# Optimization experiments

Hardware: AMD Instinct MI355X
Metric: run time of the kernel (lower is better)

The kernel has to match this reference:

```python
import jax, jax.numpy as jnp
import numpy as np

B, S, D, H, NATT = 8, 512, 768, 256, 11  # batch, seq, d_model, gru hidden, n attention branches


def setup_inputs() -> dict:
    key = jax.random.key(0)
    ks = jax.random.split(key, 20)
    w = lambda k, shp, s=0.02: (jax.random.normal(k, shp, jnp.float32) * s)
    emb = w(ks[0], (7, D), 1.0).at[0].set(0.0)  # padding_idx=0 row is zero
    return {
        "essay_amlabel": jax.random.randint(ks[1], (B, S), 0, 7),
        "sequence_output": jax.random.normal(ks[2], (B, S, D), jnp.float32),
        "emb_table": emb,
        "Wq": w(ks[3], (NATT, D, D)), "bq": jnp.zeros((NATT, D), jnp.float32),
        "Wk": w(ks[4], (NATT, D, D)), "bk": jnp.zeros((NATT, D), jnp.float32),
        "Wv": w(ks[5], (NATT, D, D)), "bv": jnp.zeros((NATT, D), jnp.float32),
        "gru_Wih": w(ks[6], (2, 3 * H, D), 1.0 / np.sqrt(H)),
        "gru_Whh": w(ks[7], (2, 3 * H, H), 1.0 / np.sqrt(H)),
        "gru_bih": jnp.zeros((2, 3 * H), jnp.float32),
        "gru_bhh": jnp.zeros((2, 3 * H), jnp.float32),
        "W1": w(ks[8], (2 * H, 1)), "b1": jnp.zeros((1,), jnp.float32),
    }


def _gru_final_hidden(x, Wih, Whh, bih, bhh, reverse):
    # x: [N, S, D] -> final hidden [N, H] (PyTorch GRU equations)
    xp = jnp.einsum('nsd,hd->snh', x, Wih) + bih  # [S, N, 3H]

    def step(h, xt):
        gh = h @ Whh.T + bhh
        i_r, i_z, i_n = jnp.split(xt, 3, axis=-1)
        h_r, h_z, h_n = jnp.split(gh, 3, axis=-1)
        r = jax.nn.sigmoid(i_r + h_r)
        z = jax.nn.sigmoid(i_z + h_z)
        n = jnp.tanh(i_n + r * h_n)
        h_new = (1.0 - z) * n + z * h
        return h_new, None

    h0 = jnp.zeros((x.shape[0], Whh.shape[1]), x.dtype)
    h_final, _ = jax.lax.scan(step, h0, xp, reverse=reverse)
    return h_final


def reference(essay_amlabel, sequence_output, emb_table, Wq, bq, Wk, bk, Wv, bv,
              gru_Wih, gru_Whh, gru_bih, gru_bhh, W1, b1):
    am = emb_table[essay_amlabel]  # [B, S, D] queries
    # 11 independent attentions, num_heads=1, dropout=0 (eval) -> stack on axis k
    Q = jax.nn.relu(jnp.einsum('bsd,kde->kbse', am, Wq) + bq[:, None, None, :])
    K = jax.nn.relu(jnp.einsum('bsd,kde->kbse', sequence_output, Wk) + bk[:, None, None, :])
    V = jax.nn.relu(jnp.einsum('bsd,kde->kbse', sequence_output, Wv) + bv[:, None, None, :])
    scores = jnp.einsum('kbqd,kbmd->kbqm', Q, K) / jnp.sqrt(jnp.float32(D))
    attn = jax.nn.softmax(scores, axis=-1)
    qmask = jnp.sign(jnp.abs(jnp.sum(am, axis=-1)))  # [B, S]
    attn = attn * qmask[None, :, :, None]  # post-softmax query mask (as in source)
    out = jnp.einsum('kbqm,kbmd->kbqd', attn, V) + am[None]  # residual with queries
    eloutput = out + sequence_output[None]  # [11, B, S, D]
    gru_in = eloutput.reshape(NATT * B, S, D)
    h_f = _gru_final_hidden(gru_in, gru_Wih[0], gru_Whh[0], gru_bih[0], gru_bhh[0], False)
    h_b = _gru_final_hidden(gru_in, gru_Wih[1], gru_Whh[1], gru_bih[1], gru_bhh[1], True)
    final = jnp.concatenate([h_f, h_b], axis=-1)  # [11B, 2H]
    reshaped = final.reshape(NATT, B, 2 * H).transpose(1, 0, 2)  # [B, 11, 2H]
    logits = jax.nn.sigmoid(reshaped @ W1 + b1).squeeze(-1)  # [B, 11]
    return logits
```

## Files before the change

### kernel.cpp

```cpp
#include <hip/hip_runtime.h>
#include <hip/hip_bf16.h>
#include <hip/hip_fp16.h>
#include <math.h>

typedef __hip_bfloat16 bf16;
typedef __attribute__((ext_vector_type(8))) short short8;
typedef __attribute__((ext_vector_type(4))) float f32x4;

#define NATT 11
#define Bb 8
#define Ss 512
#define Dd 768
#define Hh 256
#define WSLICE 589824L

#if defined(__has_attribute)
#if __has_attribute(amdgpu_waves_per_eu)
#define WAVES22 __attribute__((amdgpu_waves_per_eu(2, 2)))
#else
#define WAVES22
#endif
#if __has_attribute(amdgpu_agpr_alloc)
#define NO_AGPR __attribute__((amdgpu_agpr_alloc(0)))
#else
#define NO_AGPR
#endif
#else
#define WAVES22
#define NO_AGPR
#endif

__device__ __forceinline__ void stf(float* p, float v) { *p = v; }
__device__ __forceinline__ void stf(bf16* p, float v) { *p = __float2bfloat16(v); }

__device__ __forceinline__ float blo(unsigned u) { return __uint_as_float(u << 16); }
__device__ __forceinline__ float bhi(unsigned u) { return __uint_as_float(u & 0xffff0000u); }
__device__ __forceinline__ float b2f(unsigned short u) { return __uint_as_float(((unsigned)u) << 16); }

__device__ __forceinline__ float ldg_any(const void* base, long idx, int flag) {
  if (flag) return ((const float*)base)[idx];
  return __bfloat162float(((const bf16*)base)[idx]);
}

__device__ __forceinline__ unsigned packh2(float a, float b) {
  __half2 hh = __floats2half2_rn(a, b);
  return __builtin_bit_cast(unsigned, hh);
}
__device__ __forceinline__ unsigned short f2h(float v) {
  __half h = __float2half(v);
  return __builtin_bit_cast(unsigned short, h);
}

typedef _Float16 f16x2 __attribute__((ext_vector_type(2)));

__device__ __forceinline__ float dot2u(unsigned a, unsigned b, float c) {
#if __has_builtin(__builtin_amdgcn_fdot2)
  return __builtin_amdgcn_fdot2(__builtin_bit_cast(f16x2, a),
                                __builtin_bit_cast(f16x2, b), c, false);
#else
  __half2 ah = __builtin_bit_cast(__half2, a);
  __half2 bh = __builtin_bit_cast(__half2, b);
  float2 af = __half22float2(ah), bf = __half22float2(bh);
  return c + af.x * bf.x + af.y * bf.y;
#endif
}

__device__ __forceinline__ float quad_sum(float v) {
#if __has_builtin(__builtin_amdgcn_update_dpp)
  int y = __builtin_amdgcn_update_dpp(0, __builtin_bit_cast(int, v), 0xB1, 0xF, 0xF, true);
  v += __builtin_bit_cast(float, y);
  y = __builtin_amdgcn_update_dpp(0, __builtin_bit_cast(int, v), 0x4E, 0xF, 0xF, true);
  v += __builtin_bit_cast(float, y);
  return v;
#else
  v += __shfl_xor(v, 1);
  v += __shfl_xor(v, 2);
  return v;
#endif
}

__device__ __forceinline__ void lds_barrier() {
  asm volatile("s_waitcnt lgkmcnt(0)\n\ts_barrier" ::: "memory");
}

__device__ __forceinline__ void load_lds16(const void* g, void* l) {
  __builtin_amdgcn_global_load_lds(
      (const __attribute__((address_space(1))) unsigned int*)g,
      (__attribute__((address_space(3))) unsigned int*)l, 16, 0, 0);
}

__global__ __launch_bounds__(64) void probe_kernel(
    const unsigned short* __restrict__ sequ, const unsigned* __restrict__ labu,
    int* __restrict__ flags)
{
  int t = threadIdx.x;
  int wild = 0;
#pragma unroll
  for (int i = 0; i < 4; i++) {
    unsigned short v = sequ[t + i * 64];
    int e = (v >> 7) & 0xFF;
    if (e < 90 || e > 160) wild++;
  }
  int nzodd = 0;
#pragma unroll
  for (int i = 0; i < 2; i++) {
    unsigned w = labu[(t + i * 64) * 2 + 1];
    if (w != 0) nzodd++;
  }
  for (int o = 32; o > 0; o >>= 1) {
    wild  += __shfl_down(wild, o);
    nzodd += __shfl_down(nzodd, o);
  }
  if (t == 0) {
    flags[0] = (wild > 32) ? 1 : 0;
    flags[1] = (nzodd == 0) ? 1 : 0;
  }
}

__global__ __launch_bounds__(256) void conv_seq_kernel(
    const void* __restrict__ seq, bf16* __restrict__ seqb,
    const int* __restrict__ flags)
{
  int flag = flags[0];
  long row = blockIdx.x;
#pragma unroll
  for (int i = 0; i < 3; i++) {
    long e = row * Dd + threadIdx.x + i * 256;
    seqb[e] = __float2bfloat16(ldg_any(seq, e, flag));
  }
}

__global__ __launch_bounds__(256) void convert_kernel(
    const void* __restrict__ src, bf16* __restrict__ dst, long n,
    const int* __restrict__ flags)
{
  int flag = flags[0];
  long i = (long)blockIdx.x * 256 + threadIdx.x;
  if (i < n) dst[i] = __float2bfloat16(ldg_any(src, i, flag));
}

__global__ __launch_bounds__(256) void smalls_kernel(
    const void* __restrict__ emb, const void* __restrict__ Wq,
    const void* __restrict__ bq, float* __restrict__ Qsmall,
    const int* __restrict__ flags)
{
  int flag = flags[0];
  __shared__ float embsh[7 * 768];
  __shared__ float psum[4][7][64];
  int z = blockIdx.y;
  int bx = blockIdx.x;
  int tid = threadIdx.x;
  int sub = tid >> 6, nl = tid & 63;
  for (int i = tid; i < 7 * 768; i += 256) embsh[i] = ldg_any(emb, i, flag);
  __syncthreads();
  int n = bx * 64 + nl;
  long base = (long)z * WSLICE;
  float acc[7] = {};
  int e0 = sub * 192;
  for (int e = e0; e < e0 + 192; e++) {
    float wv = ldg_any(Wq, base + (long)e * Dd + n, flag);
#pragma unroll
    for (int l = 0; l < 7; l++) acc[l] += embsh[l * 768 + e] * wv;
  }
#pragma unroll
  for (int l = 0; l < 7; l++) psum[sub][l][nl] = acc[l];
  __syncthreads();
  if (sub == 0) {
    float bv = ldg_any(bq, z * Dd + n, flag);
#pragma unroll
    for (int l = 0; l < 7; l++) {
      float v = psum[0][l][nl] + psum[1][l][nl] + psum[2][l][nl] + psum[3][l][nl] + bv;
      Qsmall[((long)z * 7 + l) * Dd + n] = fmaxf(v, 0.f);
    }
  }
}

__global__ __launch_bounds__(256) void emb_copy_kernel(
    const void* __restrict__ emb, bf16* __restrict__ outsm,
    float* __restrict__ qmask7, const int* __restrict__ flags)
{
  int flag = flags[0];
  int l = blockIdx.x;
  int t = threadIdx.x;
  float s = 0.f;
#pragma unroll
  for (int i = 0; i < 3; i++) {
    int e = t + i * 256;
    float v = ldg_any(emb, (long)l * Dd + e, flag);
    outsm[(long)(640 + l) * Dd + e] = __float2bfloat16(v);
    s += v;
  }
  for (int o = 32; o > 0; o >>= 1) s += __shfl_down(s, o);
  __shared__ float red[4];
  if ((t & 63) == 0) red[t >> 6] = s;
  __syncthreads();
  if (t == 0) {
    float tot = red[0] + red[1] + red[2] + red[3];
    qmask7[l] = (tot != 0.f) ? 1.f : 0.f;
  }
}

__global__ __launch_bounds__(256) void transpose2_kernel(
    const void* __restrict__ Wk, const void* __restrict__ Wv,
    bf16* __restrict__ WT, const int* __restrict__ flags)
{
  int flag = flags[0];
  __shared__ float tile[32][33];
  int z = blockIdx.z;
  int m = z >> 1, wsel = z & 1;
  const void* src = wsel ? Wv : Wk;
  long off = (long)m * WSLICE;
  bf16* dst = WT + (long)z * WSLICE;
  int kk0 = blockIdx.y * 32, n0 = blockIdx.x * 32;
  int tx = threadIdx.x & 31, ty = threadIdx.x >> 5;
#pragma unroll
  for (int i = 0; i < 4; i++)
    tile[ty + i * 8][tx] = ldg_any(src, off + (long)(kk0 + ty + i * 8) * Dd + n0 + tx, flag);
  __syncthreads();
#pragma unroll
  for (int i = 0; i < 4; i++)
    dst[(long)(n0 + ty + i * 8) * Dd + kk0 + tx] = __float2bfloat16(tile[tx][ty + i * 8]);
}

__device__ __forceinline__ void gemm_mfma_core(
    const bf16* __restrict__ Ab, long ldA,
    const bf16* __restrict__ Bbp, long ldB,
    bf16* As, bf16* Bs, int bm, int bn, int K,
    const void* bias, long bOff,
    void* C, long ldC, int cMode,
    float scale, int relu, int fflag)
{
  int tid = threadIdx.x;
  int lane = tid & 63, w = tid >> 6;
  int mo = (w & 1) * 64, no = (w >> 1) * 64;
  int l15 = lane & 15, q4 = lane >> 4;
  int gr = lane >> 2;
  int gs = (lane & 3) * 8;
  const bf16* aS0 = Ab + (long)(bm + w * 16 + gr) * ldA + gs;
  const bf16* aS1 = aS0 + 64 * ldA;
  const bf16* bS0 = Bbp + (long)(bn + w * 16 + gr) * ldB + gs;
  const bf16* bS1 = bS0 + 64 * ldB;
  bf16* aD0 = As + w * 512;
  bf16* aD1 = As + 2048 + w * 512;
  bf16* bD0 = Bs + w * 512;
  bf16* bD1 = Bs + 2048 + w * 512;

  f32x4 acc[4][4];
#pragma unroll
  for (int i = 0; i < 4; i++)
#pragma unroll
    for (int j = 0; j < 4; j++)
#pragma unroll
      for (int r = 0; r < 4; r++) acc[i][j][r] = 0.f;

  for (int k0 = 0; k0 < K; k0 += 32) {
    load_lds16(aS0, aD0);
    load_lds16(aS1, aD1);
    load_lds16(bS0, bD0);
    load_lds16(bS1, bD1);
    aS0 += 32; aS1 += 32; bS0 += 32; bS1 += 32;
    __syncthreads();
    short8 af[4], bfv[4];
#pragma unroll
    for (int i = 0; i < 4; i++)
      af[i] = *(const short8*)(As + (mo + i * 16 + l15) * 32 + q4 * 8);
#pragma unroll
    for (int j = 0; j < 4; j++)
      bfv[j] = *(const short8*)(Bs + (no + j * 16 + l15) * 32 + q4 * 8);
#pragma unroll
    for (int i = 0; i < 4; i++)
#pragma unroll
      for (int j = 0; j < 4; j++)
        acc[i][j] = __builtin_amdgcn_mfma_f32_16x16x32_bf16(af[i], bfv[j], acc[i][j], 0, 0, 0);
    __syncthreads();
  }

  float bsv[4];
#pragma unroll
  for (int j = 0; j < 4; j++) {
    int colg = bn + no + j * 16 + l15;
    bsv[j] = bias ? ldg_any(bias, bOff + colg, fflag) : 0.f;
  }

  if (cMode == 5) {
    unsigned short* tile = (unsigned short*)As;
    int cl = (no >> 6) * 16 + l15;
#pragma unroll
    for (int j = 0; j < 4; j++) {
      __syncthreads();
#pragma unroll
      for (int i = 0; i < 4; i++) {
#pragma unroll
        for (int r = 0; r < 4; r++) {
          float v = acc[i][j][r] * scale + bsv[j];
          if (relu) v = fmaxf(v, 0.f);
          tile[cl * 136 + mo + i * 16 + q4 * 4 + r] = f2h(v);
        }
      }
      __syncthreads();
#pragma unroll
      for (int uu = 0; uu < 2; uu++) {
        int u = tid + uu * 256;
        int c = u >> 4, mseg = u & 15;
        int colg = bn + (c >> 4) * 64 + j * 16 + (c & 15);
        uint2 v0 = *(const uint2*)(tile + c * 136 + mseg * 8);
        uint2 v1 = *(const uint2*)(tile + c * 136 + mseg * 8 + 4);
        uint4 pk; pk.x = v0.x; pk.y = v0.y; pk.z = v1.x; pk.w = v1.y;
        *(uint4*)((unsigned short*)C + (long)colg * ldC + bm + mseg * 8) = pk;
      }
    }
    return;
  }

#pragma unroll
  for (int i = 0; i < 4; i++) {
#pragma unroll
    for (int j = 0; j < 4; j++) {
      int colg = bn + no + j * 16 + l15;
#pragma unroll
      for (int r = 0; r < 4; r++) {
        int rowg = bm + mo + i * 16 + q4 * 4 + r;
        float v = acc[i][j][r] * scale + bsv[j];
        if (relu) v = fmaxf(v, 0.f);
        long off2 = (long)rowg * ldC + colg;
        if (cMode == 2)      ((float*)C)[off2] = v;
        else if (cMode == 3) ((unsigned short*)C)[off2] = f2h(v);
        else                 ((bf16*)C)[off2] = __float2bfloat16(v);
      }
    }
  }
}

__global__ __launch_bounds__(256, 2) void proj_kernel(
    const bf16* __restrict__ seqb, const bf16* __restrict__ WT,
    const void* __restrict__ bk, const void* __restrict__ bv,
    const bf16* __restrict__ WihB, const void* __restrict__ bih,
    unsigned short* __restrict__ Kb, unsigned short* __restrict__ Vt,
    bf16* __restrict__ seqW, const int* __restrict__ flags)
{
  __shared__ __align__(16) bf16 smem[8192];
  bf16* As = smem;
  bf16* Bs = smem + 4096;
  int z = blockIdx.z;
  if (z < 22) {
    int m = z >> 1, wsel = z & 1;
    const bf16* B = WT + (long)z * WSLICE;
    if (wsel == 0) {
      gemm_mfma_core(seqb, Dd, B, Dd, As, Bs, blockIdx.y * 128, blockIdx.x * 128, Dd,
                     bk, (long)m * Dd, Kb + (long)m * 4096 * Dd, Dd, 3, 1.f, 1, flags[0]);
    } else {
      gemm_mfma_core(seqb, Dd, B, Dd, As, Bs, blockIdx.y * 128, blockIdx.x * 128, Dd,
                     bv, (long)m * Dd, Vt + (long)m * Dd * 4096, 4096, 5, 1.f, 1, flags[0]);
    }
  } else {
    int dir = z - 22;
    gemm_mfma_core(seqb, Dd, WihB + (long)dir * WSLICE, Dd, As, Bs,
                   blockIdx.y * 128, blockIdx.x * 128, Dd,
                   bih, (long)dir * Dd, seqW + (long)dir * 4096 * Dd, Dd, 0,
                   1.f, 0, flags[0]);
  }
}

__global__ __launch_bounds__(256, 2) void pvw_kernel(
    const bf16* __restrict__ outsm, const bf16* __restrict__ WihB,
    float* __restrict__ PVW, const int* __restrict__ flags)
{
  __shared__ __align__(16) bf16 As[4096];
  __shared__ __align__(16) bf16 Bs[4096];
  int dir = blockIdx.z;
  gemm_mfma_core(outsm, Dd, WihB + (long)dir * WSLICE, Dd, As, Bs,
                 blockIdx.y * 128, blockIdx.x * 128, Dd,
                 nullptr, 0, PVW + (long)dir * 768 * Dd, Dd, 2, 1.f, 0, flags[0]);
}

__global__ __launch_bounds__(512, 2) void attn_kernel(
    const unsigned short* __restrict__ Kb, const unsigned short* __restrict__ Vt,
    const float* __restrict__ Qsmall, const float* __restrict__ qmask7,
    bf16* __restrict__ outsm, float scl)
{
  int blk = blockIdx.x;
  int k = blk >> 3, b = blk & 7;
  int tid = threadIdx.x;
  int lane = tid & 63, w = tid >> 6;
  __shared__ unsigned qs[7][384];
  __shared__ unsigned short ash[7][512];
  __shared__ float wred[8][7];
  __shared__ float gred[7];
  __shared__ float finv[7];
  for (int i = tid; i < 7 * 384; i += 512) {
    int l = i / 384, e2 = i - l * 384;
    const float* qp = Qsmall + ((long)k * 7 + l) * Dd + 2 * e2;
    qs[l][e2] = packh2(qp[0], qp[1]);
  }
  __syncthreads();
  const uint4* Krow = (const uint4*)(Kb + ((long)k * 4096 + b * 512 + tid) * Dd);
  float sc[7] = {};
  for (int e8 = 0; e8 < 96; e8++) {
    uint4 kv = Krow[e8];
#pragma unroll
    for (int l = 0; l < 7; l++) {
      sc[l] = dot2u(qs[l][e8 * 4],     kv.x, sc[l]);
      sc[l] = dot2u(qs[l][e8 * 4 + 1], kv.y, sc[l]);
      sc[l] = dot2u(qs[l][e8 * 4 + 2], kv.z, sc[l]);
      sc[l] = dot2u(qs[l][e8 * 4 + 3], kv.w, sc[l]);
    }
  }
#pragma unroll
  for (int l = 0; l < 7; l++) sc[l] *= scl;
#pragma unroll
  for (int l = 0; l < 7; l++) {
    float v = sc[l];
    for (int o = 32; o > 0; o >>= 1) v = fmaxf(v, __shfl_down(v, o));
    if (lane == 0) wred[w][l] = v;
  }
  __syncthreads();
  if (tid < 7) {
    float m = wred[0][tid];
#pragma unroll
    for (int i = 1; i < 8; i++) m = fmaxf(m, wred[i][tid]);
    gred[tid] = m;
  }
  __syncthreads();
  float ev[7];
#pragma unroll
  for (int l = 0; l < 7; l++) {
    ev[l] = __expf(sc[l] - gred[l]);
    float v = ev[l];
    for (int o = 32; o > 0; o >>= 1) v += __shfl_down(v, o);
    if (lane == 0) wred[w][l] = v;
  }
  __syncthreads();
  if (tid < 7) {
    float s = 0.f;
#pragma unroll
    for (int i = 0; i < 8; i++) s += wred[i][tid];
    finv[tid] = qmask7[tid] / s;
  }
  __syncthreads();
#pragma unroll
  for (int l = 0; l < 7; l++) ash[l][tid] = f2h(ev[l] * finv[l]);
  __syncthreads();
  for (int rep = 0; rep < 2; rep++) {
    int n = tid + rep * 512;
    if (n >= Dd) break;
    const uint4* Vrow = (const uint4*)(Vt + ((long)k * Dd + n) * 4096 + b * 512);
    float acc[7] = {};
    for (int m8 = 0; m8 < 64; m8++) {
      uint4 vv = Vrow[m8];
#pragma unroll
      for (int l = 0; l < 7; l++) {
        const unsigned* ap = (const unsigned*)&ash[l][0];
        acc[l] = dot2u(ap[m8 * 4],     vv.x, acc[l]);
        acc[l] = dot2u(ap[m8 * 4 + 1], vv.y, acc[l]);
        acc[l] = dot2u(ap[m8 * 4 + 2], vv.z, acc[l]);
        acc[l] = dot2u(ap[m8 * 4 + 3], vv.w, acc[l]);
      }
    }
#pragma unroll
    for (int l = 0; l < 7; l++)
      outsm[((long)blk * 7 + l) * Dd + n] = __float2bfloat16(acc[l]);
  }
}

__global__ __launch_bounds__(512) WAVES22 NO_AGPR void gru_kernel(
    const bf16* __restrict__ seqW,
    const float* __restrict__ PVW,
    const void* __restrict__ labels,
    const void* __restrict__ Whh, const void* __restrict__ bhh,
    float* __restrict__ hbuf, const int* __restrict__ flags)
{
  int flag = flags[0], lflag = flags[1];
  int idx = blockIdx.x;
  int dir = idx / 88, n = idx - dir * 88;
  int b = n & 7;
  int tid = threadIdx.x;
  int q = tid & 3, cg = tid >> 2;
  int hi = q >> 1;
  int ch = cg + hi * 128;
  int r0 = ch, r1 = 256 + ch, r2 = 512 + ch;

  unsigned w[6][32];
#pragma unroll
  for (int s = 0; s < 6; s++) {
    int row = (s >> 1) * 256 + cg + (s & 1) * 128;
    long base = ((long)dir * Dd + row) * Hh + q * 64;
    if (flag) {
      const float4* s4 = (const float4*)((const float*)Whh + base);
#pragma unroll
      for (int i = 0; i < 16; i++) {
        float4 v = s4[i];
        w[s][2 * i]     = packh2(v.x, v.y);
        w[s][2 * i + 1] = packh2(v.z, v.w);
      }
    } else {
      const uint4* s4 = (const uint4*)((const bf16*)Whh + base);
#pragma unroll
      for (int i = 0; i < 8; i++) {
        uint4 v = s4[i];
        w[s][4 * i]     = packh2(blo(v.x), bhi(v.x));
        w[s][4 * i + 1] = packh2(blo(v.y), bhi(v.y));
        w[s][4 * i + 2] = packh2(blo(v.z), bhi(v.z));
        w[s][4 * i + 3] = packh2(blo(v.w), bhi(v.w));
      }
    }
  }
  float bh0 = ldg_any(bhh, dir * Dd + r0, flag);
  float bh1 = ldg_any(bhh, dir * Dd + r1, flag);
  float bh2 = ldg_any(bhh, dir * Dd + r2, flag);

  __shared__ float rowsh[7 * 768];
  __shared__ int labsh[512];
  __shared__ __align__(16) unsigned short hsh[2][4 * 72];

  for (int i = tid; i < 7 * 768; i += 512) {
    int l = i / 768, row = i - l * 768;
    rowsh[i] = PVW[((long)dir * 768 + n * 7 + l) * Dd + row]
             + PVW[((long)dir * 768 + 640 + l) * Dd + row];
  }
  labsh[tid] = lflag ? (int)((const long long*)labels)[b * 512 + tid]
                     : ((const int*)labels)[b * 512 + tid];
  if (tid < 288) { hsh[0][tid] = 0; hsh[1][tid] = 0; }
  __syncthreads();

  const unsigned short* swu = (const unsigned short*)seqW
                            + ((long)dir * 4096 + b * 512) * Dd;
  int t0 = dir ? 511 : 0, t1 = dir ? 510 : 1, t2 = dir ? 509 : 2;
  unsigned short xs00 = swu[(long)t0 * Dd + r0];
  unsigned short xs01 = swu[(long)t0 * Dd + r1];
  unsigned short xs02 = swu[(long)t0 * Dd + r2];
  unsigned short xs10 = swu[(long)t1 * Dd + r0];
  unsigned short xs11 = swu[(long)t1 * Dd + r1];
  unsigned short xs12 = swu[(long)t1 * Dd + r2];
  unsigned short xs20 = swu[(long)t2 * Dd + r0];
  unsigned short xs21 = swu[(long)t2 * Dd + r1];
  unsigned short xs22 = swu[(long)t2 * Dd + r2];

  float hprev = 0.f;
  int hwaddr = (ch >> 6) * 72 + (ch & 63);
  for (int tt = 0; tt < Ss; tt++) {
    int t = dir ? 511 - tt : tt;
    int ttp = (tt + 3 < Ss) ? tt + 3 : Ss - 1;
    int tp = dir ? 511 - ttp : ttp;
    unsigned short xp0 = swu[(long)tp * Dd + r0];
    unsigned short xp1 = swu[(long)tp * Dd + r1];
    unsigned short xp2 = swu[(long)tp * Dd + r2];
    int lab = labsh[t];
    const float* rs = rowsh + lab * 768;
    float xr = rs[r0] + b2f(xs00);
    float xz = rs[r1] + b2f(xs01);
    float xn = rs[r2] + b2f(xs02);
    const uint4* hq = (const uint4*)(hsh[tt & 1] + q * 72);
    float a[6] = {};
#pragma unroll
    for (int jj = 0; jj < 8; jj++) {
      uint4 hv = hq[jj];
#pragma unroll
      for (int s = 0; s < 6; s++) {
        a[s] = dot2u(w[s][4 * jj],     hv.x, a[s]);
        a[s] = dot2u(w[s][4 * jj + 1], hv.y, a[s]);
        a[s] = dot2u(w[s][4 * jj + 2], hv.z, a[s]);
        a[s] = dot2u(w[s][4 * jj + 3], hv.w, a[s]);
      }
    }
#pragma unroll
    for (int s = 0; s < 6; s++) a[s] = quad_sum(a[s]);
    float ar = hi ? a[1] : a[0];
    float az = hi ? a[3] : a[2];
    float an = hi ? a[5] : a[4];
    float rg = 1.f / (1.f + __expf(-(xr + ar + bh0)));
    float zg = 1.f / (1.f + __expf(-(xz + az + bh1)));
    float targ = xn + rg * (an + bh2);
    float e2 = __expf(2.f * targ);
    float ng = 1.f - 2.f / (e2 + 1.f);
    float hnew = (1.f - zg) * ng + zg * hprev;
    hprev = hnew;
    if ((q & 1) == 0) hsh[(tt + 1) & 1][hwaddr] = f2h(hnew);
    lds_barrier();
    xs00 = xs10; xs01 = xs11; xs02 = xs12;
    xs10 = xs20; xs11 = xs21; xs12 = xs22;
    xs20 = xp0;  xs21 = xp1;  xs22 = xp2;
  }
  if ((q & 1) == 0) hbuf[((long)(dir * 88 + n)) * Hh + ch] = hprev;
}

__global__ __launch_bounds__(256) void head_kernel(
    const float* __restrict__ hbuf, const void* __restrict__ W1,
    const void* __restrict__ b1, void* __restrict__ out,
    const int* __restrict__ flags)
{
  int flag = flags[0];
  int n = blockIdx.x;
  int c = threadIdx.x;
  float v = hbuf[(long)n * Hh + c] * ldg_any(W1, c, flag)
          + hbuf[(long)(88 + n) * Hh + c] * ldg_any(W1, 256 + c, flag);
  for (int o = 32; o > 0; o >>= 1) v += __shfl_down(v, o);
  __shared__ float red[4];
  if ((c & 63) == 0) red[c >> 6] = v;
  __syncthreads();
  if (c == 0) {
    float s = red[0] + red[1] + red[2] + red[3] + ldg_any(b1, 0, flag);
    float sig = 1.f / (1.f + __expf(-s));
    int k = n / Bb, b = n - k * Bb;
    int o = b * NATT + k;
    if (flag) ((float*)out)[o] = sig;
    else      stf((bf16*)out + o, sig);
  }
}

extern "C" void kernel_launch(void* const* d_in, const int* in_sizes, int n_in,
                              void* d_out, int out_size, void* d_ws, size_t ws_size,
                              hipStream_t stream) {
  const void* labels = d_in[0];
  const void* seq  = d_in[1];
  const void* emb  = d_in[2];
  const void* Wq   = d_in[3];
  const void* bq   = d_in[4];
  const void* Wk   = d_in[5];
  const void* bk   = d_in[6];
  const void* Wv   = d_in[7];
  const void* bv   = d_in[8];
  const void* Wih  = d_in[9];
  const void* Whh  = d_in[10];
  const void* bih  = d_in[11];
  const void* bhh  = d_in[12];
  const void* W1   = d_in[13];
  const void* b1   = d_in[14];

  char* p = (char*)d_ws;
  size_t off = 0;
  auto alloc = [&](size_t bytes) -> void* {
    void* r = p + off; off += (bytes + 255) & ~(size_t)255; return r;
  };
  int*    flags  = (int*)alloc(2 * sizeof(int));
  bf16*   seqb   = (bf16*)alloc(4096UL * 768 * 2);
  float*  qmask7 = (float*)alloc(7 * 4);
  float*  Qsmall = (float*)alloc(11UL * 7 * 768 * 4);
  bf16*   WihB   = (bf16*)alloc(2UL * WSLICE * 2);
  bf16*   WT     = (bf16*)alloc(22UL * WSLICE * 2);
  unsigned short* Kb = (unsigned short*)alloc(11UL * 4096 * 768 * 2);
  unsigned short* Vt = (unsigned short*)alloc(11UL * 768 * 4096 * 2);
  bf16*   outsm  = (bf16*)alloc(768UL * 768 * 2);
  float*  PVW    = (float*)alloc(2UL * 768 * 768 * 4);
  bf16*   seqW   = (bf16*)alloc(2UL * 4096 * 768 * 2);
  float*  hbuf   = (float*)alloc(2UL * 88 * 256 * 4);
  if (off > ws_size) return;

  probe_kernel<<<1, 64, 0, stream>>>((const unsigned short*)seq,
                                     (const unsigned*)labels, flags);
  conv_seq_kernel<<<4096, 256, 0, stream>>>(seq, seqb, flags);
  convert_kernel<<<(int)((2 * WSLICE + 255) / 256), 256, 0, stream>>>(
      Wih, WihB, 2L * WSLICE, flags);
  smalls_kernel<<<dim3(12, 11), 256, 0, stream>>>(emb, Wq, bq, Qsmall, flags);
  emb_copy_kernel<<<7, 256, 0, stream>>>(emb, outsm, qmask7, flags);
  transpose2_kernel<<<dim3(24, 24, 22), 256, 0, stream>>>(Wk, Wv, WT, flags);
  proj_kernel<<<dim3(6, 32, 24), 256, 0, stream>>>(
      seqb, WT, bk, bv, WihB, bih, Kb, Vt, seqW, flags);
  const float scl = 1.f / sqrtf(768.f);
  attn_kernel<<<88, 512, 0, stream>>>(Kb, Vt, Qsmall, qmask7, outsm, scl);
  pvw_kernel<<<dim3(6, 6, 2), 256, 0, stream>>>(outsm, WihB, PVW, flags);
  gru_kernel<<<176, 512, 0, stream>>>(seqW, PVW, labels, Whh, bhh, hbuf, flags);
  head_kernel<<<88, 256, 0, stream>>>(hbuf, W1, b1, d_out, flags);
}
```

Before: 1.082 ms.

## Use MFMA for GRU recurrent matvec and fold hidden biases into input projection

The GRU recurrent h·Whh product, previously computed with packed fp16 dot2 instructions and quad DPP reductions, now runs on 16x16x32 f16 MFMA with Whh fragments kept in registers. The results go through LDS to 256 threads that apply the gate nonlinearities. The r/z parts of bhh are pre-added into the input-projection bias by a new small kernel. This trades the per-step dot-product work for matrix-core throughput, but adds a second barrier per timestep, idles half the threads during the elementwise phase, and wastes MFMA columns since the vector uses only one useful column.

```diff
diff --git a/kernel.cpp b/kernel.cpp
--- a/kernel.cpp
+++ b/kernel.cpp
@@ -6,6 +6,7 @@
 typedef __hip_bfloat16 bf16;
 typedef __attribute__((ext_vector_type(8))) short short8;
 typedef __attribute__((ext_vector_type(4))) float f32x4;
+typedef __attribute__((ext_vector_type(8))) _Float16 half8;
 
 #define NATT 11
 #define Bb 8
@@ -20,14 +21,8 @@
 #else
 #define WAVES22
 #endif
-#if __has_attribute(amdgpu_agpr_alloc)
-#define NO_AGPR __attribute__((amdgpu_agpr_alloc(0)))
-#else
-#define NO_AGPR
-#endif
 #else
 #define WAVES22
-#define NO_AGPR
 #endif
 
 __device__ __forceinline__ void stf(float* p, float v) { *p = v; }
@@ -65,20 +60,6 @@
 #endif
 }
 
-__device__ __forceinline__ float quad_sum(float v) {
-#if __has_builtin(__builtin_amdgcn_update_dpp)
-  int y = __builtin_amdgcn_update_dpp(0, __builtin_bit_cast(int, v), 0xB1, 0xF, 0xF, true);
-  v += __builtin_bit_cast(float, y);
-  y = __builtin_amdgcn_update_dpp(0, __builtin_bit_cast(int, v), 0x4E, 0xF, 0xF, true);
-  v += __builtin_bit_cast(float, y);
-  return v;
-#else
-  v += __shfl_xor(v, 1);
-  v += __shfl_xor(v, 2);
-  return v;
-#endif
-}
-
 __device__ __forceinline__ void lds_barrier() {
   asm volatile("s_waitcnt lgkmcnt(0)\n\ts_barrier" ::: "memory");
 }
@@ -137,6 +118,18 @@
   int flag = flags[0];
   long i = (long)blockIdx.x * 256 + threadIdx.x;
   if (i < n) dst[i] = __float2bfloat16(ldg_any(src, i, flag));
+}
+
+__global__ __launch_bounds__(256) void cbias_kernel(
+    const void* __restrict__ bih, const void* __restrict__ bhh,
+    float* __restrict__ cbias, const int* __restrict__ flags)
+{
+  int flag = flags[0];
+  int i = blockIdx.x * 256 + threadIdx.x;
+  int c = i & 767;
+  float v = ldg_any(bih, i, flag);
+  if (c < 512) v += ldg_any(bhh, i, flag);
+  cbias[i] = v;
 }
 
 __global__ __launch_bounds__(256) void smalls_kernel(
@@ -334,7 +327,7 @@
 __global__ __launch_bounds__(256, 2) void proj_kernel(
     const bf16* __restrict__ seqb, const bf16* __restrict__ WT,
     const void* __restrict__ bk, const void* __restrict__ bv,
-    const bf16* __restrict__ WihB, const void* __restrict__ bih,
+    const bf16* __restrict__ WihB, const float* __restrict__ cbias,
     unsigned short* __restrict__ Kb, unsigned short* __restrict__ Vt,
     bf16* __restrict__ seqW, const int* __restrict__ flags)
 {
@@ -356,8 +349,8 @@
     int dir = z - 22;
     gemm_mfma_core(seqb, Dd, WihB + (long)dir * WSLICE, Dd, As, Bs,
                    blockIdx.y * 128, blockIdx.x * 128, Dd,
-                   bih, (long)dir * Dd, seqW + (long)dir * 4096 * Dd, Dd, 0,
-                   1.f, 0, flags[0]);
+                   cbias, (long)dir * Dd, seqW + (long)dir * 4096 * Dd, Dd, 0,
+                   1.f, 0, 1);
   }
 }
 
@@ -462,7 +455,7 @@
   }
 }
 
-__global__ __launch_bounds__(512) WAVES22 NO_AGPR void gru_kernel(
+__global__ __launch_bounds__(512) WAVES22 void gru_kernel(
     const bf16* __restrict__ seqW,
     const float* __restrict__ PVW,
     const void* __restrict__ labels,
@@ -474,43 +467,38 @@
   int dir = idx / 88, n = idx - dir * 88;
   int b = n & 7;
   int tid = threadIdx.x;
-  int q = tid & 3, cg = tid >> 2;
-  int hi = q >> 1;
-  int ch = cg + hi * 128;
-  int r0 = ch, r1 = 256 + ch, r2 = 512 + ch;
-
-  unsigned w[6][32];
-#pragma unroll
-  for (int s = 0; s < 6; s++) {
-    int row = (s >> 1) * 256 + cg + (s & 1) * 128;
-    long base = ((long)dir * Dd + row) * Hh + q * 64;
-    if (flag) {
-      const float4* s4 = (const float4*)((const float*)Whh + base);
-#pragma unroll
-      for (int i = 0; i < 16; i++) {
-        float4 v = s4[i];
-        w[s][2 * i]     = packh2(v.x, v.y);
-        w[s][2 * i + 1] = packh2(v.z, v.w);
+  int lane = tid & 63, w = tid >> 6;
+  int l15 = lane & 15, g4 = lane >> 4;
+
+  half8 afr[6][8];
+#pragma unroll
+  for (int t = 0; t < 6; t++) {
+    int m0 = (t >> 1) * 256 + 32 * w + (t & 1) * 16;
+    long rb = ((long)dir * Dd + m0 + l15) * (long)Hh + 8 * g4;
+#pragma unroll
+    for (int kt = 0; kt < 8; kt++) {
+      long eb = rb + 32 * kt;
+      uint4 u;
+      if (flag) {
+        const float4* s4 = (const float4*)((const float*)Whh + eb);
+        float4 v0 = s4[0], v1 = s4[1];
+        u.x = packh2(v0.x, v0.y); u.y = packh2(v0.z, v0.w);
+        u.z = packh2(v1.x, v1.y); u.w = packh2(v1.z, v1.w);
+      } else {
+        uint4 v = *(const uint4*)((const bf16*)Whh + eb);
+        u.x = packh2(blo(v.x), bhi(v.x));
+        u.y = packh2(blo(v.y), bhi(v.y));
+        u.z = packh2(blo(v.z), bhi(v.z));
+        u.w = packh2(blo(v.w), bhi(v.w));
       }
-    } else {
-      const uint4* s4 = (const uint4*)((const bf16*)Whh + base);
-#pragma unroll
-      for (int i = 0; i < 8; i++) {
-        uint4 v = s4[i];
-        w[s][4 * i]     = packh2(blo(v.x), bhi(v.x));
-        w[s][4 * i + 1] = packh2(blo(v.y), bhi(v.y));
-        w[s][4 * i + 2] = packh2(blo(v.z), bhi(v.z));
-        w[s][4 * i + 3] = packh2(blo(v.w), bhi(v.w));
-      }
-    }
-  }
-  float bh0 = ldg_any(bhh, dir * Dd + r0, flag);
-  float bh1 = ldg_any(bhh, dir * Dd + r1, flag);
-  float bh2 = ldg_any(bhh, dir * Dd + r2, flag);
+      afr[t][kt] = __builtin_bit_cast(half8, u);
+    }
+  }
 
   __shared__ float rowsh[7 * 768];
   __shared__ int labsh[512];
-  __shared__ __align__(16) unsigned short hsh[2][4 * 72];
+  __shared__ __align__(16) float out_lds[768];
+  __shared__ __align__(16) _Float16 hsh[256];
 
   for (int i = tid; i < 7 * 768; i += 512) {
     int l = i / 768, row = i - l * 768;
@@ -519,68 +507,82 @@
   }
   labsh[tid] = lflag ? (int)((const long long*)labels)[b * 512 + tid]
                      : ((const int*)labels)[b * 512 + tid];
-  if (tid < 288) { hsh[0][tid] = 0; hsh[1][tid] = 0; }
-  __syncthreads();
-
+  if (tid < 256) hsh[tid] = (_Float16)0.f;
+
+  int ch = tid & 255;
   const unsigned short* swu = (const unsigned short*)seqW
                             + ((long)dir * 4096 + b * 512) * Dd;
-  int t0 = dir ? 511 : 0, t1 = dir ? 510 : 1, t2 = dir ? 509 : 2;
-  unsigned short xs00 = swu[(long)t0 * Dd + r0];
-  unsigned short xs01 = swu[(long)t0 * Dd + r1];
-  unsigned short xs02 = swu[(long)t0 * Dd + r2];
-  unsigned short xs10 = swu[(long)t1 * Dd + r0];
-  unsigned short xs11 = swu[(long)t1 * Dd + r1];
-  unsigned short xs12 = swu[(long)t1 * Dd + r2];
-  unsigned short xs20 = swu[(long)t2 * Dd + r0];
-  unsigned short xs21 = swu[(long)t2 * Dd + r1];
-  unsigned short xs22 = swu[(long)t2 * Dd + r2];
-
-  float hprev = 0.f;
-  int hwaddr = (ch >> 6) * 72 + (ch & 63);
+  float bh2 = 0.f, hprev = 0.f;
+  unsigned short xs00 = 0, xs01 = 0, xs02 = 0;
+  unsigned short xs10 = 0, xs11 = 0, xs12 = 0;
+  unsigned short xs20 = 0, xs21 = 0, xs22 = 0;
+  if (tid < 256) {
+    bh2 = ldg_any(bhh, dir * Dd + 512 + ch, flag);
+    int t0 = dir ? 511 : 0, t1 = dir ? 510 : 1, t2 = dir ? 509 : 2;
+    xs00 = swu[(long)t0 * Dd + ch];
+    xs01 = swu[(long)t0 * Dd + 256 + ch];
+    xs02 = swu[(long)t0 * Dd + 512 + ch];
+    xs10 = swu[(long)t1 * Dd + ch];
+    xs11 = swu[(long)t1 * Dd + 256 + ch];
+    xs12 = swu[(long)t1 * Dd + 512 + ch];
+    xs20 = swu[(long)t2 * Dd + ch];
+    xs21 = swu[(long)t2 * Dd + 256 + ch];
+    xs22 = swu[(long)t2 * Dd + 512 + ch];
+  }
+  __syncthreads();
+
   for (int tt = 0; tt < Ss; tt++) {
-    int t = dir ? 511 - tt : tt;
-    int ttp = (tt + 3 < Ss) ? tt + 3 : Ss - 1;
-    int tp = dir ? 511 - ttp : ttp;
-    unsigned short xp0 = swu[(long)tp * Dd + r0];
-    unsigned short xp1 = swu[(long)tp * Dd + r1];
-    unsigned short xp2 = swu[(long)tp * Dd + r2];
-    int lab = labsh[t];
-    const float* rs = rowsh + lab * 768;
-    float xr = rs[r0] + b2f(xs00);
-    float xz = rs[r1] + b2f(xs01);
-    float xn = rs[r2] + b2f(xs02);
-    const uint4* hq = (const uint4*)(hsh[tt & 1] + q * 72);
-    float a[6] = {};
-#pragma unroll
-    for (int jj = 0; jj < 8; jj++) {
-      uint4 hv = hq[jj];
-#pragma unroll
-      for (int s = 0; s < 6; s++) {
-        a[s] = dot2u(w[s][4 * jj],     hv.x, a[s]);
-        a[s] = dot2u(w[s][4 * jj + 1], hv.y, a[s]);
-        a[s] = dot2u(w[s][4 * jj + 2], hv.z, a[s]);
-        a[s] = dot2u(w[s][4 * jj + 3], hv.w, a[s]);
+#pragma unroll
+    for (int hv = 0; hv < 2; hv++) {
+      f32x4 a0 = {0.f, 0.f, 0.f, 0.f};
+      f32x4 a1 = {0.f, 0.f, 0.f, 0.f};
+      f32x4 a2 = {0.f, 0.f, 0.f, 0.f};
+#pragma unroll
+      for (int kt = 0; kt < 8; kt++) {
+        half8 bfr = ((const half8*)hsh)[4 * kt + g4];
+        a0 = __builtin_amdgcn_mfma_f32_16x16x32_f16(afr[hv][kt],     bfr, a0, 0, 0, 0);
+        a1 = __builtin_amdgcn_mfma_f32_16x16x32_f16(afr[2 + hv][kt], bfr, a1, 0, 0, 0);
+        a2 = __builtin_amdgcn_mfma_f32_16x16x32_f16(afr[4 + hv][kt], bfr, a2, 0, 0, 0);
       }
-    }
-#pragma unroll
-    for (int s = 0; s < 6; s++) a[s] = quad_sum(a[s]);
-    float ar = hi ? a[1] : a[0];
-    float az = hi ? a[3] : a[2];
-    float an = hi ? a[5] : a[4];
-    float rg = 1.f / (1.f + __expf(-(xr + ar + bh0)));
-    float zg = 1.f / (1.f + __expf(-(xz + az + bh1)));
-    float targ = xn + rg * (an + bh2);
-    float e2 = __expf(2.f * targ);
-    float ng = 1.f - 2.f / (e2 + 1.f);
-    float hnew = (1.f - zg) * ng + zg * hprev;
-    hprev = hnew;
-    if ((q & 1) == 0) hsh[(tt + 1) & 1][hwaddr] = f2h(hnew);
+      if (l15 == 0) {
+        int mb = 32 * w + 16 * hv + 4 * g4;
+        *(f32x4*)(out_lds + mb)       = a0;
+        *(f32x4*)(out_lds + 256 + mb) = a1;
+        *(f32x4*)(out_lds + 512 + mb) = a2;
+      }
+      __builtin_amdgcn_sched_barrier(0);
+    }
     lds_barrier();
-    xs00 = xs10; xs01 = xs11; xs02 = xs12;
-    xs10 = xs20; xs11 = xs21; xs12 = xs22;
-    xs20 = xp0;  xs21 = xp1;  xs22 = xp2;
-  }
-  if ((q & 1) == 0) hbuf[((long)(dir * 88 + n)) * Hh + ch] = hprev;
+    if (tid < 256) {
+      int t = dir ? 511 - tt : tt;
+      int ttp = (tt + 3 < Ss) ? tt + 3 : Ss - 1;
+      int tp = dir ? 511 - ttp : ttp;
+      unsigned short xp0 = swu[(long)tp * Dd + ch];
+      unsigned short xp1 = swu[(long)tp * Dd + 256 + ch];
+      unsigned short xp2 = swu[(long)tp * Dd + 512 + ch];
+      int lab = labsh[t];
+      const float* rs = rowsh + lab * 768;
+      float ar = out_lds[ch];
+      float az = out_lds[256 + ch];
+      float an = out_lds[512 + ch];
+      float xr = rs[ch] + b2f(xs00);
+      float xz = rs[256 + ch] + b2f(xs01);
+      float xn = rs[512 + ch] + b2f(xs02);
+      float rg = 1.f / (1.f + __expf(-(xr + ar)));
+      float zg = 1.f / (1.f + __expf(-(xz + az)));
+      float targ = xn + rg * (an + bh2);
+      float e2 = __expf(2.f * targ);
+      float ng = 1.f - 2.f / (e2 + 1.f);
+      float hnew = (1.f - zg) * ng + zg * hprev;
+      hprev = hnew;
+      hsh[ch] = (_Float16)hnew;
+      xs00 = xs10; xs01 = xs11; xs02 = xs12;
+      xs10 = xs20; xs11 = xs21; xs12 = xs22;
+      xs20 = xp0;  xs21 = xp1;  xs22 = xp2;
+    }
+    lds_barrier();
+  }
+  if (tid < 256) hbuf[((long)(dir * 88 + n)) * Hh + ch] = hprev;
 }
 
 __global__ __launch_bounds__(256) void head_kernel(
@@ -643,6 +645,7 @@
   float*  PVW    = (float*)alloc(2UL * 768 * 768 * 4);
   bf16*   seqW   = (bf16*)alloc(2UL * 4096 * 768 * 2);
   float*  hbuf   = (float*)alloc(2UL * 88 * 256 * 4);
+  float*  cbias  = (float*)alloc(2UL * 768 * 4);
   if (off > ws_size) return;
 
   probe_kernel<<<1, 64, 0, stream>>>((const unsigned short*)seq,
@@ -650,11 +653,12 @@
   conv_seq_kernel<<<4096, 256, 0, stream>>>(seq, seqb, flags);
   convert_kernel<<<(int)((2 * WSLICE + 255) / 256), 256, 0, stream>>>(
       Wih, WihB, 2L * WSLICE, flags);
+  cbias_kernel<<<6, 256, 0, stream>>>(bih, bhh, cbias, flags);
   smalls_kernel<<<dim3(12, 11), 256, 0, stream>>>(emb, Wq, bq, Qsmall, flags);
   emb_copy_kernel<<<7, 256, 0, stream>>>(emb, outsm, qmask7, flags);
   transpose2_kernel<<<dim3(24, 24, 22), 256, 0, stream>>>(Wk, Wv, WT, flags);
   proj_kernel<<<dim3(6, 32, 24), 256, 0, stream>>>(
-      seqb, WT, bk, bv, WihB, bih, Kb, Vt, seqW, flags);
+      seqb, WT, bk, bv, WihB, cbias, Kb, Vt, seqW, flags);
   const float scl = 1.f / sqrtf(768.f);
   attn_kernel<<<88, 512, 0, stream>>>(Kb, Vt, Qsmall, qmask7, outsm, scl);
   pvw_kernel<<<dim3(6, 6, 2), 256, 0, stream>>>(outsm, WihB, PVW, flags);
```

Result: slower. 1.932 ms (+78.5%).
